# Optimization experiments

Hardware: AMD Instinct MI355X
Metric: run time of the kernel (lower is better)

The kernel has to match this reference:

```python
import jax, jax.numpy as jnp
import numpy as np

N, E, C, L = 50000, 625000, 128, 4
H = 2 * C  # hidden size of per-layer ObjectModel
FRAC_SCALE = 1.0 / 16.0   # fractional_bitwidth = 4
Q_MAX = 8.0               # int_bitwidth = 4 -> signed fixed point range [-8, 8 - 1/16]


def fq(x):
    """Fixed-point fake-quantize (4 int bits, 4 frac bits, signed)."""
    return jnp.clip(jnp.round(x / FRAC_SCALE) * FRAC_SCALE, -Q_MAX, Q_MAX - FRAC_SCALE)


def qlin(h, W, b):
    # QuantLinear: input/weight/bias/output all quantized
    return fq(fq(h) @ fq(W) + fq(b))


def qbn(h, w, b):
    # BatchNorm1dToQuantScaleBias in inference: per-channel scale + bias
    return fq(fq(h) * fq(w) + fq(b))


def setup_inputs() -> dict:
    key = jax.random.key(0)
    ks = jax.random.split(key, 24)
    d = {}
    d["x"] = jax.random.normal(ks[0], (N, 3), dtype=jnp.float32)
    d["edge_attr"] = jax.random.normal(ks[1], (E, 4), dtype=jnp.float32)
    d["edge_index"] = jax.random.randint(ks[2], (2, E), 0, N, dtype=jnp.int64)
    # encoders
    d["node_W"] = jax.random.normal(ks[3], (3, C), dtype=jnp.float32) * 0.4
    d["node_b"] = jax.random.normal(ks[4], (C,), dtype=jnp.float32) * 0.2
    d["edge_W"] = jax.random.normal(ks[5], (4, C), dtype=jnp.float32) * 0.4
    d["edge_b"] = jax.random.normal(ks[6], (C,), dtype=jnp.float32) * 0.2
    d["node_bn_w"] = 1.0 + 0.1 * jax.random.normal(ks[7], (C,), dtype=jnp.float32)
    d["node_bn_b"] = 0.1 * jax.random.normal(ks[8], (C,), dtype=jnp.float32)
    d["edge_bn_w"] = 1.0 + 0.1 * jax.random.normal(ks[9], (C,), dtype=jnp.float32)
    d["edge_bn_b"] = 0.1 * jax.random.normal(ks[10], (C,), dtype=jnp.float32)
    # per-layer ObjectModel params (stacked over L)
    d["W1"] = jax.random.normal(ks[11], (L, C, H), dtype=jnp.float32) * (0.5 / np.sqrt(C))
    d["b1"] = jax.random.normal(ks[12], (L, H), dtype=jnp.float32) * 0.1
    d["bn_w"] = 1.0 + 0.1 * jax.random.normal(ks[13], (L, H), dtype=jnp.float32)
    d["bn_b"] = 0.1 * jax.random.normal(ks[14], (L, H), dtype=jnp.float32)
    d["W2"] = jax.random.normal(ks[15], (L, H, C), dtype=jnp.float32) * (0.5 / np.sqrt(H))
    d["b2"] = jax.random.normal(ks[16], (L, C), dtype=jnp.float32) * 0.1
    d["fc_W"] = jax.random.normal(ks[17], (C, 1), dtype=jnp.float32) * (0.5 / np.sqrt(C))
    d["fc_b"] = jax.random.normal(ks[18], (1,), dtype=jnp.float32) * 0.1
    return d


def reference(x, edge_attr, edge_index, node_W, node_b, edge_W, edge_b,
              node_bn_w, node_bn_b, edge_bn_w, edge_bn_b,
              W1, b1, bn_w, bn_b, W2, b2, fc_W, fc_b):
    src = edge_index[0]  # x_j (source) under flow='source_to_target'
    tgt = edge_index[1]  # aggregation target i

    h = fq(qlin(x, node_W, node_b))            # node encoder [N, C]
    e = fq(qlin(edge_attr, edge_W, edge_b))    # edge encoder [E, C]
    h = qbn(h, node_bn_w, node_bn_b)
    e = qbn(e, edge_bn_w, edge_bn_b)

    for l in range(L):
        # message: quant(x_j) + quant(edge_attr), QuantReLU
        msg = fq(jax.nn.relu(fq(h[src]) + fq(e)))          # [E, C]
        agg = jax.ops.segment_sum(msg, tgt, num_segments=N)  # scatter-sum [N, C]
        u = fq(agg)
        # ObjectModel: QuantLinear -> ScaleBias BN -> QuantReLU -> QuantLinear, then QuantIdentity
        z = qlin(u, W1[l], b1[l])
        z = qbn(z, bn_w[l], bn_b[l])
        z = fq(jax.nn.relu(z))
        z = fq(qlin(z, W2[l], b2[l]))
        h = h + z                                           # residual

    pooled = jnp.mean(h, axis=0, keepdims=True)  # global_mean_pool, batch=None -> [1, C]
    out = qlin(fq(pooled), fc_W, fc_b)           # [1, 1]
    out = fq(jax.nn.sigmoid(fq(out)))            # QuantSigmoid
    return out.reshape(-1)                       # [1]
```

## Files before the change

kernel.cpp:

```cpp
#include <hip/hip_runtime.h>
#include <stdint.h>

#define NN 50000
#define EE 625000
#define EPAD (EE + 16)
#define CC 128
#define HH 256
#define LL 4
#define NPAD 50048
#define NBLK (NPAD/64)
#define R2 32

typedef __attribute__((ext_vector_type(4))) int   i32x4;
typedef __attribute__((ext_vector_type(4))) float f32x4;

__device__ __forceinline__ float qbf(float x){
  return fminf(127.f, fmaxf(-128.f, rintf(x*16.f)));
}
__device__ __forceinline__ float rq16(float t){
  return fminf(127.f, fmaxf(-128.f, rintf(t*0.0625f)));
}

__global__ void k_qbig(const float* __restrict__ W1, const float* __restrict__ W2,
                       signed char* __restrict__ w1q8, signed char* __restrict__ w2q8){
  int i = blockIdx.x*256 + threadIdx.x;
  if (i >= LL*CC*HH) return;
  {
    float v = qbf(W1[i]);
    int l = i / (CC*HH); int r = i - l*CC*HH; int c = r / HH; int hh = r - c*HH;
    w1q8[((size_t)l*HH + hh)*CC + c] = (signed char)v;
  }
  {
    float v = qbf(W2[i]);
    int l = i / (HH*CC); int r = i - l*HH*CC; int hh = r / CC; int c = r - hh*CC;
    w2q8[((size_t)l*CC + c)*HH + hh] = (signed char)v;
  }
}

struct QS { const float* s; float* d; int n; float m; };
struct QSArgs { QS q[14]; };

__global__ void k_qsmall(QSArgs a){
  for (int r=0;r<14;++r){
    QS qs = a.q[r];
    for (int i = blockIdx.x*blockDim.x + threadIdx.x; i < qs.n; i += gridDim.x*blockDim.x)
      qs.d[i] = qs.m * qbf(qs.s[i]);
  }
}

__global__ __launch_bounds__(256) void k_node_enc(
    const float* __restrict__ x, const float* __restrict__ nW,
    const float* __restrict__ nb16, const float* __restrict__ bnw,
    const float* __restrict__ bnb16, short* __restrict__ h0,
    signed char* __restrict__ hq8){
  int idx = blockIdx.x*256 + threadIdx.x;
  int n = idx >> 7, c = idx & 127;
  float x0 = qbf(x[n*3]), x1 = qbf(x[n*3+1]), x2 = qbf(x[n*3+2]);
  float S = x0*nW[c] + x1*nW[CC+c] + x2*nW[2*CC+c];
  float v1 = rq16(S + nb16[c]);
  float v2 = rq16(v1*bnw[c] + bnb16[c]);
  h0[idx] = (short)v2;
  hq8[idx] = (signed char)v2;
}

__global__ void k_deg(const int* __restrict__ ei, int* __restrict__ deg){
  int e = blockIdx.x*256 + threadIdx.x;
  if (e < EE) atomicAdd(&deg[ei[EE + e]], 1);
}

__global__ __launch_bounds__(256) void k_scanA(const int* __restrict__ deg,
                                               int* __restrict__ offI,
                                               int* __restrict__ btot){
  __shared__ int sh[256];
  int t = threadIdx.x;
  int base = blockIdx.x*1024 + t*4;
  int v[4]; int s = 0;
  #pragma unroll
  for (int i=0;i<4;++i){ v[i] = (base+i < NN) ? deg[base+i] : 0; s += v[i]; }
  sh[t] = s; __syncthreads();
  for (int off=1; off<256; off<<=1){
    int xv = (t>=off) ? sh[t-off] : 0;
    __syncthreads();
    sh[t] += xv;
    __syncthreads();
  }
  int run = (t>0) ? sh[t-1] : 0;
  #pragma unroll
  for (int i=0;i<4;++i){ run += v[i]; if (base+i < NN) offI[base+i] = run; }
  if (t==255) btot[blockIdx.x] = sh[255];
}

__global__ void k_scanB(const int* __restrict__ btot, int* __restrict__ boff, int nblk){
  if (threadIdx.x==0 && blockIdx.x==0){
    int run = 0;
    for (int b=0;b<nblk;++b){ int v = btot[b]; boff[b] = run; run += v; }
  }
}

__global__ void k_scanC(const int* __restrict__ boff, const int* __restrict__ deg,
                        int* __restrict__ offI, int* __restrict__ cursor){
  int i = blockIdx.x*256 + threadIdx.x;
  if (i < NN){
    int v = offI[i] + boff[i>>10];
    offI[i] = v;
    cursor[i] = v - deg[i];
  }
}

__global__ void k_fill(const int* __restrict__ ei, const float* __restrict__ ea,
                       int* __restrict__ cursor, int* __restrict__ srcoff,
                       int* __restrict__ qpk){
  int e = blockIdx.x*256 + threadIdx.x;
  if (e < EE){
    int tgt = ei[EE + e];
    int p = atomicAdd(&cursor[tgt], 1);
    srcoff[p] = ei[e] * CC;
    float4 v = ((const float4*)ea)[e];
    int b0 = (int)qbf(v.x) & 0xff, b1 = (int)qbf(v.y) & 0xff;
    int b2 = (int)qbf(v.z) & 0xff, b3 = (int)qbf(v.w) & 0xff;
    qpk[p] = b0 | (b1<<8) | (b2<<16) | (b3<<24);
  }
}

__global__ __launch_bounds__(256) void k_eenc(
    const int* __restrict__ qpk,
    const float* __restrict__ ewf, const float* __restrict__ eb16,
    const float* __restrict__ ebnw, const float* __restrict__ ebnb16,
    signed char* __restrict__ eq){
  int t = blockIdx.x*256 + threadIdx.x;
  int c0 = (t & 31) * 4;
  float wv0[4], wv1[4], wv2[4], wv3[4], ebv[4], bwv[4], bbv[4];
  #pragma unroll
  for (int j=0;j<4;++j){
    int c = c0 + j;
    wv0[j]=ewf[c]; wv1[j]=ewf[CC+c]; wv2[j]=ewf[2*CC+c]; wv3[j]=ewf[3*CC+c];
    ebv[j]=eb16[c]; bwv[j]=ebnw[c]; bbv[j]=ebnb16[c];
  }
  int stride = (gridDim.x*256) >> 5;
  for (int p = t >> 5; p < EE; p += stride){
    int q = qpk[p];
    float qx = (float)(int)(signed char)(q & 0xff);
    float qy = (float)(int)(signed char)((q>>8) & 0xff);
    float qz = (float)(int)(signed char)((q>>16) & 0xff);
    float qw = (float)(int)(signed char)(q>>24);
    uint packed = 0;
    #pragma unroll
    for (int j=0;j<4;++j){
      float S  = qx*wv0[j] + qy*wv1[j] + qz*wv2[j] + qw*wv3[j];
      float v1 = rq16(S + ebv[j]);
      float ec = rq16(v1*bwv[j] + bbv[j]);
      packed |= ((uint)((int)ec & 0xff)) << (8*j);
    }
    *(uint*)(eq + ((size_t)p << 7) + c0) = packed;
  }
}

template<int PRE>
__global__ __launch_bounds__(256) void k_msg(
    const int* __restrict__ offI, const int* __restrict__ deg_,
    const int* __restrict__ srcoff, const int* __restrict__ qpk,
    const signed char* __restrict__ eq,
    const float* __restrict__ ewf, const float* __restrict__ eb16,
    const float* __restrict__ ebnw, const float* __restrict__ ebnb16,
    const signed char* __restrict__ hq8, signed char* __restrict__ uq){
  int n = blockIdx.x*4 + (threadIdx.x >> 6);
  int lane = threadIdx.x & 63;
  int c0 = lane*2;
  float w0a,w1a,w2a,w3a,eba,bwa,bba, w0b,w1b,w2b,w3b,ebb,bwb,bbb;
  if (!PRE){
    w0a=ewf[c0];   w1a=ewf[CC+c0];   w2a=ewf[2*CC+c0];   w3a=ewf[3*CC+c0];
    eba=eb16[c0];  bwa=ebnw[c0];     bba=ebnb16[c0];
    w0b=ewf[c0+1]; w1b=ewf[CC+c0+1]; w2b=ewf[2*CC+c0+1]; w3b=ewf[3*CC+c0+1];
    ebb=eb16[c0+1];bwb=ebnw[c0+1];   bbb=ebnb16[c0+1];
  }
  int end = offI[n];
  int start = end - deg_[n];
  int acc0 = 0, acc1 = 0;
  for (int base = start; base < end; base += 16){
    int rem = end - base;
    int so = srcoff[base + min(lane, rem-1)];
    ushort hv[16], ev[16];
    #pragma unroll
    for (int j=0;j<16;++j){
      int soj = __builtin_amdgcn_readlane(so, j);
      hv[j] = *(const ushort*)(hq8 + soj + c0);
      if (PRE) ev[j] = *(const ushort*)(eq + (((size_t)(base+j)) << 7) + c0);
    }
    #pragma unroll
    for (int j=0;j<16;++j){
      if (j < rem){
        int h0 = ((int)hv[j] << 24) >> 24;
        int h1 = ((int)(short)hv[j]) >> 8;
        int e0, e1;
        if (PRE){
          e0 = ((int)ev[j] << 24) >> 24;
          e1 = ((int)(short)ev[j]) >> 8;
        } else {
          int q = qpk[base+j];
          float qx = (float)(int)(signed char)(q & 0xff);
          float qy = (float)(int)(signed char)((q>>8) & 0xff);
          float qz = (float)(int)(signed char)((q>>16) & 0xff);
          float qw = (float)(int)(signed char)(q>>24);
          float Sa = qx*w0a + qy*w1a + qz*w2a + qw*w3a;
          float Sb = qx*w0b + qy*w1b + qz*w2b + qw*w3b;
          e0 = (int)rq16(rq16(Sa + eba)*bwa + bba);
          e1 = (int)rq16(rq16(Sb + ebb)*bwb + bbb);
        }
        acc0 += min(max(h0 + e0, 0), 127);
        acc1 += min(max(h1 + e1, 0), 127);
      }
    }
  }
  int ua = min(acc0, 127), ub = min(acc1, 127);
  *(ushort*)(uq + (size_t)n*CC + c0) = (ushort)((ua & 0xff) | ((ub & 0xff) << 8));
}

__global__ __launch_bounds__(256, 3) void k_om(
    int l, const signed char* __restrict__ uq,
    const signed char* __restrict__ w1q8, const float* __restrict__ b1q16,
    const float* __restrict__ bnwf, const float* __restrict__ bnb16,
    const signed char* __restrict__ w2q8, const float* __restrict__ b2q16,
    const short* __restrict__ h_in, short* __restrict__ h_out,
    signed char* __restrict__ hq8, int* __restrict__ partial){
  __shared__ signed char uL[64][144];
  __shared__ signed char zL[64][272];
  int t = threadIdx.x;
  int nb = blockIdx.x * 64;
  {
    const i32x4* src = (const i32x4*)(uq + (size_t)nb*CC + t*32);
    int flat = t*32; int r = flat >> 7, c = flat & 127;
    *(i32x4*)&uL[r][c]      = src[0];
    *(i32x4*)&uL[r][c + 16] = src[1];
  }
  int lane = t & 63, wv = t >> 6;
  int lr = lane & 15, lk = lane >> 4;
  const signed char* W1p = w1q8 + (size_t)l*HH*CC;
  i32x4 w1f[2][4];
  #pragma unroll
  for (int ks=0; ks<2; ++ks)
    #pragma unroll
    for (int ci=0; ci<4; ++ci)
      w1f[ks][ci] = *(const i32x4*)(W1p + (size_t)(wv*64 + ci*16 + lr)*CC + ks*64 + lk*16);
  __syncthreads();

  i32x4 acc[4][4];
  #pragma unroll
  for (int mi=0;mi<4;++mi)
    #pragma unroll
    for (int ci=0;ci<4;++ci) acc[mi][ci] = (i32x4){0,0,0,0};
  #pragma unroll
  for (int ks=0; ks<2; ++ks){
    i32x4 av[4];
    #pragma unroll
    for (int mi=0;mi<4;++mi) av[mi] = *(const i32x4*)&uL[mi*16+lr][ks*64 + lk*16];
    #pragma unroll
    for (int mi=0;mi<4;++mi)
      #pragma unroll
      for (int ci=0;ci<4;++ci)
        acc[mi][ci] = __builtin_amdgcn_mfma_i32_16x16x64_i8(av[mi], w1f[ks][ci], acc[mi][ci], 0,0,0);
  }
  #pragma unroll
  for (int ci=0;ci<4;++ci){
    int hcol = wv*64 + ci*16 + lr;
    float b1 = b1q16[l*HH + hcol];
    float bw = bnwf[l*HH + hcol];
    float bb = bnb16[l*HH + hcol];
    #pragma unroll
    for (int mi=0;mi<4;++mi){
      #pragma unroll
      for (int r=0;r<4;++r){
        float v1 = rq16((float)acc[mi][ci][r] + b1);
        float v2 = fmaxf(rq16(v1*bw + bb), 0.f);
        zL[mi*16 + lk*4 + r][hcol] = (signed char)v2;
      }
    }
  }
  const signed char* W2p = w2q8 + (size_t)l*CC*HH;
  i32x4 w2f[4][2];
  #pragma unroll
  for (int ks=0; ks<4; ++ks)
    #pragma unroll
    for (int ci=0; ci<2; ++ci)
      w2f[ks][ci] = *(const i32x4*)(W2p + (size_t)(wv*32 + ci*16 + lr)*HH + ks*64 + lk*16);
  __syncthreads();

  i32x4 a2[4][2];
  #pragma unroll
  for (int mi=0;mi<4;++mi){ a2[mi][0] = (i32x4){0,0,0,0}; a2[mi][1] = (i32x4){0,0,0,0}; }
  #pragma unroll
  for (int ks=0; ks<4; ++ks){
    i32x4 av[4];
    #pragma unroll
    for (int mi=0;mi<4;++mi) av[mi] = *(const i32x4*)&zL[mi*16+lr][ks*64 + lk*16];
    #pragma unroll
    for (int mi=0;mi<4;++mi)
      #pragma unroll
      for (int ci=0;ci<2;++ci)
        a2[mi][ci] = __builtin_amdgcn_mfma_i32_16x16x64_i8(av[mi], w2f[ks][ci], a2[mi][ci], 0,0,0);
  }
  int psum[2] = {0, 0};
  #pragma unroll
  for (int ci=0;ci<2;++ci){
    int ccol = wv*32 + ci*16 + lr;
    float b2 = b2q16[l*CC + ccol];
    #pragma unroll
    for (int mi=0;mi<4;++mi){
      #pragma unroll
      for (int r=0;r<4;++r){
        int node = nb + mi*16 + lk*4 + r;
        float v = rq16((float)a2[mi][ci][r] + b2);
        int hn = (int)h_in[(size_t)node*CC + ccol] + (int)v;
        if (node < NN){
          h_out[(size_t)node*CC + ccol] = (short)hn;
          hq8[(size_t)node*CC + ccol] = (signed char)min(max(hn, -128), 127);
          psum[ci] += hn;
        }
      }
    }
  }
  if (partial){
    #pragma unroll
    for (int ci=0;ci<2;++ci){
      int s = psum[ci];
      s += __shfl_xor(s, 16);
      s += __shfl_xor(s, 32);
      if (lk == 0)
        partial[blockIdx.x*CC + wv*32 + ci*16 + lr] = s;
    }
  }
}

__global__ __launch_bounds__(256) void k_red(
    const int* __restrict__ partial, int* __restrict__ partial2){
  int t = threadIdx.x;
  int c = t & 127;
  int sub = blockIdx.x*2 + (t >> 7);
  int s = 0;
  for (int b = sub; b < NBLK; b += R2) s += partial[b*CC + c];
  partial2[sub*CC + c] = s;
}

__global__ __launch_bounds__(256) void k_final(
    const int* __restrict__ partial2, const float* __restrict__ fcwf,
    const float* __restrict__ fcb16, float* __restrict__ out){
  __shared__ int ired[128];
  __shared__ float red[128];
  int t = threadIdx.x;
  int c = t & 127, half = t >> 7;
  int s = 0;
  #pragma unroll
  for (int b = half; b < R2; b += 2) s += partial2[b*CC + c];
  if (half) ired[c] = s;
  __syncthreads();
  if (!half){
    int sc = s + ired[c];
    double m = (double)sc / (double)NN;
    float pq = fminf(127.f, fmaxf(-128.f, (float)rint(m)));
    red[c] = pq * fcwf[c];
  }
  __syncthreads();
  for (int o=64;o>0;o>>=1){ if (t<o) red[t] += red[t+o]; __syncthreads(); }
  if (t==0){
    float v = rq16(red[0] + fcb16[0]);
    float o1 = v * 0.0625f;
    float sg = 1.f/(1.f + expf(-o1));
    float oq = fminf(127.f, fmaxf(-128.f, rintf(sg*16.f)));
    out[0] = oq * 0.0625f;
  }
}

extern "C" void kernel_launch(void* const* d_in, const int* in_sizes, int n_in,
                              void* d_out, int out_size, void* d_ws, size_t ws_size,
                              hipStream_t stream){
  (void)in_sizes; (void)n_in; (void)out_size;
  const float* x   = (const float*)d_in[0];
  const float* ea  = (const float*)d_in[1];
  const int*   ei  = (const int*)d_in[2];
  const float* W1  = (const float*)d_in[11];
  const float* W2  = (const float*)d_in[15];

  char* w = (char*)d_ws;
  auto alloc = [&](size_t bytes)->char*{
    char* p = w; w += (bytes + 255) & ~(size_t)255; return p;
  };
  short* h0        = (short*)alloc((size_t)NPAD*CC*2);
  short* h1        = (short*)alloc((size_t)NPAD*CC*2);
  signed char* hq8 = (signed char*)alloc((size_t)NPAD*CC);
  signed char* uq  = (signed char*)alloc((size_t)NPAD*CC);
  int* qpk         = (int*)alloc((size_t)EPAD*4);
  int* srcoff      = (int*)alloc((size_t)EPAD*4);
  int* deg         = (int*)alloc(NN*4);
  int* offI        = (int*)alloc(NN*4);
  int* cursor      = (int*)alloc(NN*4);
  int* btot        = (int*)alloc(64*4);
  int* boff        = (int*)alloc(64*4);
  int* partial     = (int*)alloc((size_t)NBLK*CC*4);
  int* partial2    = (int*)alloc((size_t)R2*CC*4);
  signed char* w1q8= (signed char*)alloc((size_t)LL*CC*HH);
  signed char* w2q8= (signed char*)alloc((size_t)LL*CC*HH);
  float* nodeWf    = (float*)alloc(3*CC*4);
  float* nb16f     = (float*)alloc(CC*4);
  float* nbnwf     = (float*)alloc(CC*4);
  float* nbnb16f   = (float*)alloc(CC*4);
  float* ewf       = (float*)alloc(4*CC*4);
  float* eb16f     = (float*)alloc(CC*4);
  float* ebnwf     = (float*)alloc(CC*4);
  float* ebnb16f   = (float*)alloc(CC*4);
  float* b1q16f    = (float*)alloc(LL*HH*4);
  float* bnwf      = (float*)alloc(LL*HH*4);
  float* bnb16f    = (float*)alloc(LL*HH*4);
  float* b2q16f    = (float*)alloc(LL*CC*4);
  float* fcwf      = (float*)alloc(CC*4);
  float* fcb16f    = (float*)alloc(256);
  size_t base_used = (size_t)(w - (char*)d_ws);
  bool PRE = (ws_size >= base_used + (size_t)EPAD*CC + (16u<<20));
  signed char* eq  = PRE ? (signed char*)alloc((size_t)EPAD*CC) : nullptr;

  hipMemsetAsync(deg, 0, NN*4, stream);

  k_qbig<<<(LL*CC*HH + 255)/256, 256, 0, stream>>>(W1, W2, w1q8, w2q8);

  QSArgs qa;
  auto setq = [&](int r, int idx, float* d, int n, float m){
    qa.q[r].s = (const float*)d_in[idx]; qa.q[r].d = d; qa.q[r].n = n; qa.q[r].m = m;
  };
  setq(0, 3,  nodeWf,  3*CC, 1.f);
  setq(1, 4,  nb16f,   CC,   16.f);
  setq(2, 5,  ewf,     4*CC, 1.f);
  setq(3, 6,  eb16f,   CC,   16.f);
  setq(4, 7,  nbnwf,   CC,   1.f);
  setq(5, 8,  nbnb16f, CC,   16.f);
  setq(6, 9,  ebnwf,   CC,   1.f);
  setq(7, 10, ebnb16f, CC,   16.f);
  setq(8, 12, b1q16f,  LL*HH, 16.f);
  setq(9, 13, bnwf,    LL*HH, 1.f);
  setq(10,14, bnb16f,  LL*HH, 16.f);
  setq(11,16, b2q16f,  LL*CC, 16.f);
  setq(12,17, fcwf,    CC,   1.f);
  setq(13,18, fcb16f,  1,    16.f);
  k_qsmall<<<4, 256, 0, stream>>>(qa);

  k_node_enc<<<(NN*CC)/256, 256, 0, stream>>>(x, nodeWf, nb16f, nbnwf, nbnb16f, h0, hq8);
  k_deg<<<(EE+255)/256, 256, 0, stream>>>(ei, deg);
  int nblk = (NN + 1023)/1024;
  k_scanA<<<nblk, 256, 0, stream>>>(deg, offI, btot);
  k_scanB<<<1, 64, 0, stream>>>(btot, boff, nblk);
  k_scanC<<<(NN+255)/256, 256, 0, stream>>>(boff, deg, offI, cursor);
  k_fill<<<(EE+255)/256, 256, 0, stream>>>(ei, ea, cursor, srcoff, qpk);
  if (PRE)
    k_eenc<<<2048, 256, 0, stream>>>(qpk, ewf, eb16f, ebnwf, ebnb16f, eq);

  for (int l=0;l<LL;++l){
    const short* hi = (l & 1) ? h1 : h0;
    short* ho       = (l & 1) ? h0 : h1;
    if (PRE)
      k_msg<1><<<NN/4, 256, 0, stream>>>(offI, deg, srcoff, qpk, eq,
                                         ewf, eb16f, ebnwf, ebnb16f, hq8, uq);
    else
      k_msg<0><<<NN/4, 256, 0, stream>>>(offI, deg, srcoff, qpk, eq,
                                         ewf, eb16f, ebnwf, ebnb16f, hq8, uq);
    k_om<<<NBLK, 256, 0, stream>>>(l, uq, w1q8, b1q16f, bnwf, bnb16f,
                                   w2q8, b2q16f, hi, ho, hq8,
                                   (l == LL-1) ? partial : nullptr);
  }
  k_red<<<R2/2, 256, 0, stream>>>(partial, partial2);
  k_final<<<1, 256, 0, stream>>>(partial2, fcwf, fcb16f, (float*)d_out);
}
```

Before: 373.1 us.

## Fuse edge encoding into first message pass and pack src offset with edge attrs

Removes the separate edge-encoder kernel: the first message layer computes the quantized edge embedding inline and writes it to the eq buffer, and later layers read it back. Source offsets and packed quantized edge attributes are merged into one int2 array, so one load and one readlane broadcast per edge serve both. This saves a kernel launch and one full pass over E×C edge data. In exchange, the first message kernel does extra compute and scattered 2-byte stores, and the eq buffer is now always allocated with no workspace-size check.

```diff
diff --git a/kernel.cpp b/kernel.cpp
--- a/kernel.cpp
+++ b/kernel.cpp
@@ -12,7 +12,6 @@
 #define R2 32
 
 typedef __attribute__((ext_vector_type(4))) int   i32x4;
-typedef __attribute__((ext_vector_type(4))) float f32x4;
 
 __device__ __forceinline__ float qbf(float x){
   return fminf(127.f, fmaxf(-128.f, rintf(x*16.f)));
@@ -108,58 +107,22 @@
 }
 
 __global__ void k_fill(const int* __restrict__ ei, const float* __restrict__ ea,
-                       int* __restrict__ cursor, int* __restrict__ srcoff,
-                       int* __restrict__ qpk){
+                       int* __restrict__ cursor, int2* __restrict__ adjq){
   int e = blockIdx.x*256 + threadIdx.x;
   if (e < EE){
     int tgt = ei[EE + e];
     int p = atomicAdd(&cursor[tgt], 1);
-    srcoff[p] = ei[e] * CC;
     float4 v = ((const float4*)ea)[e];
     int b0 = (int)qbf(v.x) & 0xff, b1 = (int)qbf(v.y) & 0xff;
     int b2 = (int)qbf(v.z) & 0xff, b3 = (int)qbf(v.w) & 0xff;
-    qpk[p] = b0 | (b1<<8) | (b2<<16) | (b3<<24);
-  }
-}
-
-__global__ __launch_bounds__(256) void k_eenc(
-    const int* __restrict__ qpk,
-    const float* __restrict__ ewf, const float* __restrict__ eb16,
-    const float* __restrict__ ebnw, const float* __restrict__ ebnb16,
-    signed char* __restrict__ eq){
-  int t = blockIdx.x*256 + threadIdx.x;
-  int c0 = (t & 31) * 4;
-  float wv0[4], wv1[4], wv2[4], wv3[4], ebv[4], bwv[4], bbv[4];
-  #pragma unroll
-  for (int j=0;j<4;++j){
-    int c = c0 + j;
-    wv0[j]=ewf[c]; wv1[j]=ewf[CC+c]; wv2[j]=ewf[2*CC+c]; wv3[j]=ewf[3*CC+c];
-    ebv[j]=eb16[c]; bwv[j]=ebnw[c]; bbv[j]=ebnb16[c];
-  }
-  int stride = (gridDim.x*256) >> 5;
-  for (int p = t >> 5; p < EE; p += stride){
-    int q = qpk[p];
-    float qx = (float)(int)(signed char)(q & 0xff);
-    float qy = (float)(int)(signed char)((q>>8) & 0xff);
-    float qz = (float)(int)(signed char)((q>>16) & 0xff);
-    float qw = (float)(int)(signed char)(q>>24);
-    uint packed = 0;
-    #pragma unroll
-    for (int j=0;j<4;++j){
-      float S  = qx*wv0[j] + qy*wv1[j] + qz*wv2[j] + qw*wv3[j];
-      float v1 = rq16(S + ebv[j]);
-      float ec = rq16(v1*bwv[j] + bbv[j]);
-      packed |= ((uint)((int)ec & 0xff)) << (8*j);
-    }
-    *(uint*)(eq + ((size_t)p << 7) + c0) = packed;
-  }
-}
-
-template<int PRE>
+    adjq[p] = make_int2(ei[e] * CC, b0 | (b1<<8) | (b2<<16) | (b3<<24));
+  }
+}
+
+template<int FIRST>
 __global__ __launch_bounds__(256) void k_msg(
     const int* __restrict__ offI, const int* __restrict__ deg_,
-    const int* __restrict__ srcoff, const int* __restrict__ qpk,
-    const signed char* __restrict__ eq,
+    const int2* __restrict__ adjq, signed char* __restrict__ eq,
     const float* __restrict__ ewf, const float* __restrict__ eb16,
     const float* __restrict__ ebnw, const float* __restrict__ ebnb16,
     const signed char* __restrict__ hq8, signed char* __restrict__ uq){
@@ -167,7 +130,7 @@
   int lane = threadIdx.x & 63;
   int c0 = lane*2;
   float w0a,w1a,w2a,w3a,eba,bwa,bba, w0b,w1b,w2b,w3b,ebb,bwb,bbb;
-  if (!PRE){
+  if (FIRST){
     w0a=ewf[c0];   w1a=ewf[CC+c0];   w2a=ewf[2*CC+c0];   w3a=ewf[3*CC+c0];
     eba=eb16[c0];  bwa=ebnw[c0];     bba=ebnb16[c0];
     w0b=ewf[c0+1]; w1b=ewf[CC+c0+1]; w2b=ewf[2*CC+c0+1]; w3b=ewf[3*CC+c0+1];
@@ -178,13 +141,15 @@
   int acc0 = 0, acc1 = 0;
   for (int base = start; base < end; base += 16){
     int rem = end - base;
-    int so = srcoff[base + min(lane, rem-1)];
+    int2 a = adjq[base + min(lane, rem-1)];
     ushort hv[16], ev[16];
+    int qk[16];
     #pragma unroll
     for (int j=0;j<16;++j){
-      int soj = __builtin_amdgcn_readlane(so, j);
+      int soj = __builtin_amdgcn_readlane(a.x, j);
       hv[j] = *(const ushort*)(hq8 + soj + c0);
-      if (PRE) ev[j] = *(const ushort*)(eq + (((size_t)(base+j)) << 7) + c0);
+      if (FIRST) qk[j] = __builtin_amdgcn_readlane(a.y, j);
+      else       ev[j] = *(const ushort*)(eq + (((size_t)(base+j)) << 7) + c0);
     }
     #pragma unroll
     for (int j=0;j<16;++j){
@@ -192,11 +157,8 @@
         int h0 = ((int)hv[j] << 24) >> 24;
         int h1 = ((int)(short)hv[j]) >> 8;
         int e0, e1;
-        if (PRE){
-          e0 = ((int)ev[j] << 24) >> 24;
-          e1 = ((int)(short)ev[j]) >> 8;
-        } else {
-          int q = qpk[base+j];
+        if (FIRST){
+          int q = qk[j];
           float qx = (float)(int)(signed char)(q & 0xff);
           float qy = (float)(int)(signed char)((q>>8) & 0xff);
           float qz = (float)(int)(signed char)((q>>16) & 0xff);
@@ -205,6 +167,11 @@
           float Sb = qx*w0b + qy*w1b + qz*w2b + qw*w3b;
           e0 = (int)rq16(rq16(Sa + eba)*bwa + bba);
           e1 = (int)rq16(rq16(Sb + ebb)*bwb + bbb);
+          *(ushort*)(eq + (((size_t)(base+j)) << 7) + c0) =
+              (ushort)((e0 & 0xff) | ((e1 & 0xff) << 8));
+        } else {
+          e0 = ((int)ev[j] << 24) >> 24;
+          e1 = ((int)(short)ev[j]) >> 8;
         }
         acc0 += min(max(h0 + e0, 0), 127);
         acc1 += min(max(h1 + e1, 0), 127);
@@ -372,7 +339,7 @@
 extern "C" void kernel_launch(void* const* d_in, const int* in_sizes, int n_in,
                               void* d_out, int out_size, void* d_ws, size_t ws_size,
                               hipStream_t stream){
-  (void)in_sizes; (void)n_in; (void)out_size;
+  (void)in_sizes; (void)n_in; (void)out_size; (void)ws_size;
   const float* x   = (const float*)d_in[0];
   const float* ea  = (const float*)d_in[1];
   const int*   ei  = (const int*)d_in[2];
@@ -387,8 +354,7 @@
   short* h1        = (short*)alloc((size_t)NPAD*CC*2);
   signed char* hq8 = (signed char*)alloc((size_t)NPAD*CC);
   signed char* uq  = (signed char*)alloc((size_t)NPAD*CC);
-  int* qpk         = (int*)alloc((size_t)EPAD*4);
-  int* srcoff      = (int*)alloc((size_t)EPAD*4);
+  int2* adjq       = (int2*)alloc((size_t)EPAD*8);
   int* deg         = (int*)alloc(NN*4);
   int* offI        = (int*)alloc(NN*4);
   int* cursor      = (int*)alloc(NN*4);
@@ -412,9 +378,7 @@
   float* b2q16f    = (float*)alloc(LL*CC*4);
   float* fcwf      = (float*)alloc(CC*4);
   float* fcb16f    = (float*)alloc(256);
-  size_t base_used = (size_t)(w - (char*)d_ws);
-  bool PRE = (ws_size >= base_used + (size_t)EPAD*CC + (16u<<20));
-  signed char* eq  = PRE ? (signed char*)alloc((size_t)EPAD*CC) : nullptr;
+  signed char* eq  = (signed char*)alloc((size_t)EPAD*CC);
 
   hipMemsetAsync(deg, 0, NN*4, stream);
 
@@ -446,18 +410,16 @@
   k_scanA<<<nblk, 256, 0, stream>>>(deg, offI, btot);
   k_scanB<<<1, 64, 0, stream>>>(btot, boff, nblk);
   k_scanC<<<(NN+255)/256, 256, 0, stream>>>(boff, deg, offI, cursor);
-  k_fill<<<(EE+255)/256, 256, 0, stream>>>(ei, ea, cursor, srcoff, qpk);
-  if (PRE)
-    k_eenc<<<2048, 256, 0, stream>>>(qpk, ewf, eb16f, ebnwf, ebnb16f, eq);
+  k_fill<<<(EE+255)/256, 256, 0, stream>>>(ei, ea, cursor, adjq);
 
   for (int l=0;l<LL;++l){
     const short* hi = (l & 1) ? h1 : h0;
     short* ho       = (l & 1) ? h0 : h1;
-    if (PRE)
-      k_msg<1><<<NN/4, 256, 0, stream>>>(offI, deg, srcoff, qpk, eq,
+    if (l == 0)
+      k_msg<1><<<NN/4, 256, 0, stream>>>(offI, deg, adjq, eq,
                                          ewf, eb16f, ebnwf, ebnb16f, hq8, uq);
     else
-      k_msg<0><<<NN/4, 256, 0, stream>>>(offI, deg, srcoff, qpk, eq,
+      k_msg<0><<<NN/4, 256, 0, stream>>>(offI, deg, adjq, eq,
                                          ewf, eb16f, ebnwf, ebnb16f, hq8, uq);
     k_om<<<NBLK, 256, 0, stream>>>(l, uq, w1q8, b1q16f, bnwf, bnb16f,
                                    w2q8, b2q16f, hi, ho, hq8,
```

After: 360.5 us. -3.4%, faster.
